# Kernel optimization log

Measured on AMD Instinct MI355X. Metric: run time of the kernel, lower is better.

Reference implementation:

```python
import jax, jax.numpy as jnp
import numpy as np

D_MODEL = 1024
N_HEADS = 16
D_K = D_MODEL // N_HEADS
B, L = 2, 2048


def setup_inputs() -> dict:
    key = jax.random.key(0)
    ks = jax.random.split(key, 13)
    s = 0.02
    inp = {
        'query': jax.random.normal(ks[0], (B, L, D_MODEL), jnp.float32),
        'key': jax.random.normal(ks[1], (B, L, D_MODEL), jnp.float32),
        'value': jax.random.normal(ks[2], (B, L, D_MODEL), jnp.float32),
        'mask': jax.random.randint(ks[3], (1, 1, L, L), 0, 2).astype(bool),
        'W_q': jax.random.normal(ks[4], (D_MODEL, D_MODEL), jnp.float32) * s,
        'b_q': jnp.zeros((D_MODEL,), jnp.float32),
        'W_k': jax.random.normal(ks[5], (D_MODEL, D_MODEL), jnp.float32) * s,
        'b_k': jnp.zeros((D_MODEL,), jnp.float32),
        'W_v': jax.random.normal(ks[6], (D_MODEL, D_MODEL), jnp.float32) * s,
        'b_v': jnp.zeros((D_MODEL,), jnp.float32),
        'W_o': jax.random.normal(ks[7], (D_MODEL, D_MODEL), jnp.float32) * s,
        'b_o': jnp.zeros((D_MODEL,), jnp.float32),
    }
    return inp


def _split_heads(x):
    b, l, _ = x.shape
    return x.reshape(b, l, N_HEADS, D_K).transpose(0, 2, 1, 3)  # [B,H,L,dk]


def reference(query, key, value, mask, W_q, b_q, W_k, b_k, W_v, b_v, W_o, b_o):
    q = _split_heads(query @ W_q + b_q)
    k = _split_heads(key @ W_k + b_k)
    v = _split_heads(value @ W_v + b_v)
    # Unscaled attention logits [B,H,L,L] (NO 1/sqrt(dk))
    logits = jnp.einsum('bhqd,bhkd->bhqk', q, k)
    logits = jnp.where(mask, -jnp.inf, logits)
    w = jax.nn.softmax(logits, axis=-1)
    w = jnp.nan_to_num(w, nan=0.0)  # fully-masked rows -> zeros
    attended = jnp.einsum('bhqk,bhkd->bhqd', w, v)
    # dropout in eval mode = identity; combine heads
    out = attended.transpose(0, 2, 1, 3).reshape(B, L, D_MODEL)
    return out @ W_o + b_o
```

## Files before the change

kernel.cpp:

```cpp
#include <hip/hip_runtime.h>
#include <hip/hip_bf16.h>
#include <stdint.h>


typedef __bf16 bf16;
typedef __bf16 bf16x8 __attribute__((ext_vector_type(8)));
typedef float f32x4 __attribute__((ext_vector_type(4)));

#define AS1 __attribute__((address_space(1)))
#define AS3 __attribute__((address_space(3)))

__device__ __forceinline__ void g2l16(const void* g, void* l) {
    __builtin_amdgcn_global_load_lds((AS1 void*)g, (AS3 void*)l, 16, 0, 0);
}

__device__ __forceinline__ bool lane_masked(unsigned long long m) {
#if __has_builtin(__builtin_amdgcn_inverse_ballot_w64)
    return __builtin_amdgcn_inverse_ballot_w64(m);
#else
    return (m >> (threadIdx.x & 63)) & 1ull;
#endif
}

#define LOG2E 1.44269504088896f

__global__ __launch_bounds__(256) void mdetect_kernel(const unsigned int* __restrict__ w,
                                                      int* __restrict__ flag) {
    int idx = blockIdx.x * 256 + threadIdx.x;
    unsigned v = w[idx];
    int f = 0;
    if (v == 0x3F800000u) f = 2;
    else if (v > 1u) f = 1;
    unsigned long long b1 = __ballot(f & 1);
    unsigned long long b2 = __ballot(f & 2);
    if ((threadIdx.x & 63) == 0) {
        int agg = (b1 ? 1 : 0) | (b2 ? 2 : 0);
        if (agg) atomicOr(flag, agg);
    }
}

__global__ __launch_bounds__(256) void mpack_kernel(const void* __restrict__ mask,
                                                    unsigned long long* __restrict__ mb,
                                                    const int* __restrict__ flag) {
    int idx = blockIdx.x * 256 + threadIdx.x;
    int f = *flag;
    bool v;
    if (f & 2)      v = ((const float*)mask)[idx] != 0.0f;
    else if (f & 1) v = ((const unsigned char*)mask)[idx] != 0;
    else            v = ((const int*)mask)[idx] != 0;
    unsigned long long b = __ballot(v);
    if ((threadIdx.x & 63) == 0) mb[idx >> 6] = b;
}

__global__ __launch_bounds__(256) void rpack_kernel(const unsigned long long* __restrict__ mb,
                                                    unsigned long long* __restrict__ rmb) {
    int task = blockIdx.x * 4 + (threadIdx.x >> 6);
    int qg = task >> 5, kt = task & 31;
    int lane = threadIdx.x & 63, quad = lane >> 4, col = lane & 15;
    #pragma unroll
    for (int r = 0; r < 4; ++r) {
        unsigned long long wrow = mb[(size_t)(qg * 16 + quad * 4 + r) * 32 + kt];
        #pragma unroll
        for (int nt = 0; nt < 4; ++nt) {
            unsigned long long b = __ballot(((wrow >> (nt * 16 + col)) & 1ull) != 0);
            if (lane == 0) rmb[(size_t)task * 16 + r * 4 + nt] = b;
        }
    }
}

__global__ __launch_bounds__(256) void prep_kernel(
    const float* __restrict__ q, const float* __restrict__ k, const float* __restrict__ v,
    bf16* xq, bf16* xk, bf16* xv,
    const float* W0, const float* W1, const float* W2, const float* W3,
    bf16* T0, bf16* T1, bf16* T2, bf16* T3) {
    __shared__ __align__(16) bf16 t[64 * 72];
    int y = blockIdx.y;
    int tid = threadIdx.x;
    if (y < 3) {
        const float* in = (y == 0) ? q : (y == 1) ? k : v;
        bf16* out = (y == 0) ? xq : (y == 1) ? xk : xv;
        int idx = blockIdx.x * 256 + tid;
        float4 vv = ((const float4*)in)[idx];
        __align__(8) bf16 o[4];
        o[0] = (bf16)vv.x; o[1] = (bf16)vv.y; o[2] = (bf16)vv.z; o[3] = (bf16)vv.w;
        *(uint2*)(out + (size_t)idx * 4) = *(const uint2*)o;
        return;
    }
    int bx = blockIdx.x;
    if (bx >= 1024) return;
    const float* W; bf16* T;
    int wi = bx >> 8;
    if (wi == 0)      { W = W0; T = T0; }
    else if (wi == 1) { W = W1; T = T1; }
    else if (wi == 2) { W = W2; T = T2; }
    else              { W = W3; T = T3; }
    int x = bx & 255;
    int tx = x & 15, ty = x >> 4;
    int n0 = tx * 64, k0 = ty * 64;
    #pragma unroll
    for (int rr = 0; rr < 4; ++rr) {
        int idx = rr * 256 + tid;
        int r = idx >> 4, c4 = (idx & 15) * 4;
        float4 vv = *(const float4*)(W + (size_t)(k0 + r) * 1024 + n0 + c4);
        __align__(8) bf16 o[4];
        o[0] = (bf16)vv.x; o[1] = (bf16)vv.y; o[2] = (bf16)vv.z; o[3] = (bf16)vv.w;
        *(uint2*)&t[r * 72 + c4] = *(const uint2*)o;
    }
    __syncthreads();
    #pragma unroll
    for (int rr = 0; rr < 2; ++rr) {
        int idx = rr * 256 + tid;
        int n = idx >> 3, kc = (idx & 7) * 8;
        __align__(16) bf16 o[8];
        #pragma unroll
        for (int j = 0; j < 8; ++j) o[j] = t[(kc + j) * 72 + n];
        *(uint4*)(T + (size_t)(n0 + n) * 1024 + k0 + kc) = *(const uint4*)o;
    }
}

template <int MODE>
__device__ __forceinline__ void gemm128_core(const bf16* __restrict__ A,
                                             const bf16* __restrict__ Bt,
                                             const float* __restrict__ bias,
                                             void* __restrict__ Out, int bm, int bn,
                                             float scale) {
    __shared__ __align__(16) bf16 la[128 * 64];
    __shared__ __align__(16) bf16 lb[128 * 64];
    int tid = threadIdx.x;
    int w = tid >> 6, lane = tid & 63;
    int quad = lane >> 4, col = lane & 15;
    int c7 = col & 7;
    int wm = w >> 1, wn = w & 1;
    int m0 = bm * 128, n0 = bn * 128;
    f32x4 acc[4][4];
    f32x4 z = {0.f, 0.f, 0.f, 0.f};
    #pragma unroll
    for (int i = 0; i < 4; ++i)
        #pragma unroll
        for (int j = 0; j < 4; ++j) acc[i][j] = z;
    int sr = lane >> 3;
    int sg = (lane & 7) ^ sr;
    int swz0 = (quad ^ c7) * 8;
    int swz1 = ((4 + quad) ^ c7) * 8;
    for (int kt = 0; kt < 16; ++kt) {
        int kk = kt * 64;
        __syncthreads();
        #pragma unroll
        for (int i = 0; i < 4; ++i) {
            int ch = w * 4 + i;
            int row = ch * 8 + sr;
            g2l16(A + (size_t)(m0 + row) * 1024 + kk + sg * 8, &la[ch * 512]);
            g2l16(Bt + (size_t)(n0 + row) * 1024 + kk + sg * 8, &lb[ch * 512]);
        }
        __syncthreads();
        bf16x8 af[4][2], bfr[4][2];
        #pragma unroll
        for (int mt = 0; mt < 4; ++mt) {
            af[mt][0] = *(const bf16x8*)&la[(wm * 64 + mt * 16 + col) * 64 + swz0];
            af[mt][1] = *(const bf16x8*)&la[(wm * 64 + mt * 16 + col) * 64 + swz1];
        }
        #pragma unroll
        for (int nt = 0; nt < 4; ++nt) {
            bfr[nt][0] = *(const bf16x8*)&lb[(wn * 64 + nt * 16 + col) * 64 + swz0];
            bfr[nt][1] = *(const bf16x8*)&lb[(wn * 64 + nt * 16 + col) * 64 + swz1];
        }
        #pragma unroll
        for (int mt = 0; mt < 4; ++mt)
            #pragma unroll
            for (int nt = 0; nt < 4; ++nt) {
                acc[mt][nt] = __builtin_amdgcn_mfma_f32_16x16x32_bf16(
                    af[mt][0], bfr[nt][0], acc[mt][nt], 0, 0, 0);
                acc[mt][nt] = __builtin_amdgcn_mfma_f32_16x16x32_bf16(
                    af[mt][1], bfr[nt][1], acc[mt][nt], 0, 0, 0);
            }
    }
    float bia[4];
    #pragma unroll
    for (int nt = 0; nt < 4; ++nt) bia[nt] = bias[n0 + wn * 64 + nt * 16 + col];
    #pragma unroll
    for (int mt = 0; mt < 4; ++mt) {
        #pragma unroll
        for (int nt = 0; nt < 4; ++nt) {
            #pragma unroll
            for (int r = 0; r < 4; ++r) {
                int m = m0 + wm * 64 + mt * 16 + quad * 4 + r;
                int n = n0 + wn * 64 + nt * 16 + col;
                float v = (acc[mt][nt][r] + bia[nt]) * scale;
                if (MODE == 0) {
                    int b = m >> 11, l = m & 2047, h = n >> 6, d = n & 63;
                    ((bf16*)Out)[(((size_t)b * 16 + h) * 2048 + l) * 64 + d] = (bf16)v;
                } else {
                    int b = m >> 11, l = m & 2047, h = n >> 6, d = n & 63;
                    ((bf16*)Out)[(((size_t)b * 16 + h) * 64 + d) * 2048 + l] = (bf16)v;
                }
            }
        }
    }
}

__global__ __launch_bounds__(256) void qkv_kernel(
    const bf16* Xq, const bf16* Xk, const bf16* Xv,
    const bf16* Wq, const bf16* Wk, const bf16* Wv,
    const float* bq, const float* bk, const float* bv,
    bf16* Qh, bf16* Kh, bf16* Vt) {
    int y = blockIdx.y;
    int bm = blockIdx.x >> 3, bn = blockIdx.x & 7;
    if (y == 0)      gemm128_core<0>(Xq, Wq, bq, Qh, bm, bn, LOG2E);
    else if (y == 1) gemm128_core<0>(Xk, Wk, bk, Kh, bm, bn, 1.0f);
    else             gemm128_core<2>(Xv, Wv, bv, Vt, bm, bn, 1.0f);
}

__global__ __launch_bounds__(256) void ogemm_kernel(const bf16* __restrict__ A,
                                                    const bf16* __restrict__ Wt,
                                                    const float* __restrict__ bias,
                                                    float* __restrict__ Out) {
    int bm = blockIdx.x >> 3, bn = blockIdx.x & 7;
    __shared__ __align__(16) bf16 la[64 * 64];
    __shared__ __align__(16) bf16 lb[128 * 64];
    int tid = threadIdx.x;
    int w = tid >> 6, lane = tid & 63;
    int quad = lane >> 4, col = lane & 15;
    int c7 = col & 7;
    int m0 = bm * 64, n0 = bn * 128;
    f32x4 acc[4][2];
    f32x4 z = {0.f, 0.f, 0.f, 0.f};
    #pragma unroll
    for (int i = 0; i < 4; ++i) { acc[i][0] = z; acc[i][1] = z; }
    int sr = lane >> 3;
    int sg = (lane & 7) ^ sr;
    int swz0 = (quad ^ c7) * 8;
    int swz1 = ((4 + quad) ^ c7) * 8;
    for (int kt = 0; kt < 16; ++kt) {
        int kk = kt * 64;
        __syncthreads();
        #pragma unroll
        for (int i = 0; i < 2; ++i) {
            int ch = w * 2 + i;
            g2l16(A + (size_t)(m0 + ch * 8 + sr) * 1024 + kk + sg * 8, &la[ch * 512]);
        }
        #pragma unroll
        for (int i = 0; i < 4; ++i) {
            int ch = w * 4 + i;
            g2l16(Wt + (size_t)(n0 + ch * 8 + sr) * 1024 + kk + sg * 8, &lb[ch * 512]);
        }
        __syncthreads();
        bf16x8 af[4][2], bfr[2][2];
        #pragma unroll
        for (int mt = 0; mt < 4; ++mt) {
            af[mt][0] = *(const bf16x8*)&la[(mt * 16 + col) * 64 + swz0];
            af[mt][1] = *(const bf16x8*)&la[(mt * 16 + col) * 64 + swz1];
        }
        #pragma unroll
        for (int nt = 0; nt < 2; ++nt) {
            bfr[nt][0] = *(const bf16x8*)&lb[(w * 32 + nt * 16 + col) * 64 + swz0];
            bfr[nt][1] = *(const bf16x8*)&lb[(w * 32 + nt * 16 + col) * 64 + swz1];
        }
        #pragma unroll
        for (int mt = 0; mt < 4; ++mt)
            #pragma unroll
            for (int nt = 0; nt < 2; ++nt) {
                acc[mt][nt] = __builtin_amdgcn_mfma_f32_16x16x32_bf16(
                    af[mt][0], bfr[nt][0], acc[mt][nt], 0, 0, 0);
                acc[mt][nt] = __builtin_amdgcn_mfma_f32_16x16x32_bf16(
                    af[mt][1], bfr[nt][1], acc[mt][nt], 0, 0, 0);
            }
    }
    float bia[2];
    bia[0] = bias[n0 + w * 32 + col];
    bia[1] = bias[n0 + w * 32 + 16 + col];
    #pragma unroll
    for (int mt = 0; mt < 4; ++mt)
        #pragma unroll
        for (int nt = 0; nt < 2; ++nt)
            #pragma unroll
            for (int r = 0; r < 4; ++r)
                Out[(size_t)(m0 + mt * 16 + quad * 4 + r) * 1024 +
                    n0 + w * 32 + nt * 16 + col] = acc[mt][nt][r] + bia[nt];
}

__global__ __launch_bounds__(128) void attn_kernel(const bf16* __restrict__ Qh,
                                                   const bf16* __restrict__ Kh,
                                                   const bf16* __restrict__ Vt,
                                                   const unsigned long long* __restrict__ rmb,
                                                   bf16* __restrict__ att) {
    int bh = blockIdx.x, qt = blockIdx.y;
    int b = bh >> 4, h = bh & 15;
    int q0 = qt * 64;
    __shared__ __align__(16) bf16 ks[64 * 64];
    __shared__ __align__(16) bf16 vs[64 * 64];
    __shared__ __align__(16) bf16 ps[2 * 32 * 72];
    int tid = threadIdx.x;
    int w = tid >> 6, lane = tid & 63;
    int quad = lane >> 4, col = lane & 15;
    int c7 = col & 7;
    int sr = lane >> 3;
    int sg = (lane & 7) ^ sr;
    int swz0 = (quad ^ c7) * 8;
    int swz1 = ((4 + quad) ^ c7) * 8;

    int mofs = __builtin_amdgcn_readfirstlane((qt * 4 + w * 2) * 512);

    #pragma unroll
    for (int i = 0; i < 4; ++i) {
        int ch = w * 4 + i;
        g2l16(Qh + ((size_t)bh * 2048 + q0 + ch * 8 + sr) * 64 + sg * 8, &ks[ch * 512]);
    }
    __syncthreads();
    bf16x8 aq[2][2];
    #pragma unroll
    for (int mt = 0; mt < 2; ++mt) {
        aq[mt][0] = *(const bf16x8*)&ks[(w * 32 + mt * 16 + col) * 64 + swz0];
        aq[mt][1] = *(const bf16x8*)&ks[(w * 32 + mt * 16 + col) * 64 + swz1];
    }
    bf16x8 onesf;
    #pragma unroll
    for (int i = 0; i < 8; ++i) onesf[i] = (bf16)1.0f;

    f32x4 z = {0.f, 0.f, 0.f, 0.f};
    f32x4 O[2][4], R[2];
    #pragma unroll
    for (int mt = 0; mt < 2; ++mt) {
        R[mt] = z;
        #pragma unroll
        for (int i = 0; i < 4; ++i) O[mt][i] = z;
    }

    for (int kt = 0; kt < 32; ++kt) {
        __syncthreads();
        #pragma unroll
        for (int i = 0; i < 4; ++i) {
            int ch = w * 4 + i;
            int r = ch * 8 + sr;
            g2l16(Kh + ((size_t)bh * 2048 + kt * 64 + r) * 64 + sg * 8, &ks[ch * 512]);
            g2l16(Vt + ((size_t)bh * 64 + r) * 2048 + kt * 64 + sg * 8, &vs[ch * 512]);
        }
        __syncthreads();

        f32x4 s[2][4];
        #pragma unroll
        for (int nt = 0; nt < 4; ++nt) {
            s[0][nt] = z; s[1][nt] = z;
            bf16x8 bk0 = *(const bf16x8*)&ks[(nt * 16 + col) * 64 + swz0];
            s[0][nt] = __builtin_amdgcn_mfma_f32_16x16x32_bf16(aq[0][0], bk0, s[0][nt], 0, 0, 0);
            s[1][nt] = __builtin_amdgcn_mfma_f32_16x16x32_bf16(aq[1][0], bk0, s[1][nt], 0, 0, 0);
            bf16x8 bk1 = *(const bf16x8*)&ks[(nt * 16 + col) * 64 + swz1];
            s[0][nt] = __builtin_amdgcn_mfma_f32_16x16x32_bf16(aq[0][1], bk1, s[0][nt], 0, 0, 0);
            s[1][nt] = __builtin_amdgcn_mfma_f32_16x16x32_bf16(aq[1][1], bk1, s[1][nt], 0, 0, 0);
        }

        #pragma unroll
        for (int mt = 0; mt < 2; ++mt) {
            const unsigned long long* mw = rmb + mofs + mt * 512 + kt * 16;
            #pragma unroll
            for (int r = 0; r < 4; ++r) {
                #pragma unroll
                for (int nt = 0; nt < 4; ++nt) {
                    float p = __builtin_amdgcn_exp2f(s[mt][nt][r]);
                    if (lane_masked(mw[r * 4 + nt])) p = 0.0f;
                    ps[w * 2304 + (mt * 16 + quad * 4 + r) * 72 + nt * 16 + col] = (bf16)p;
                }
            }
        }

        bf16x8 ap[2][2];
        #pragma unroll
        for (int mt = 0; mt < 2; ++mt) {
            ap[mt][0] = *(const bf16x8*)&ps[w * 2304 + (mt * 16 + col) * 72 + quad * 8];
            ap[mt][1] = *(const bf16x8*)&ps[w * 2304 + (mt * 16 + col) * 72 + 32 + quad * 8];
        }
        #pragma unroll
        for (int dt = 0; dt < 4; ++dt) {
            bf16x8 bv0 = *(const bf16x8*)&vs[(dt * 16 + col) * 64 + swz0];
            O[0][dt] = __builtin_amdgcn_mfma_f32_16x16x32_bf16(ap[0][0], bv0, O[0][dt], 0, 0, 0);
            O[1][dt] = __builtin_amdgcn_mfma_f32_16x16x32_bf16(ap[1][0], bv0, O[1][dt], 0, 0, 0);
            bf16x8 bv1 = *(const bf16x8*)&vs[(dt * 16 + col) * 64 + swz1];
            O[0][dt] = __builtin_amdgcn_mfma_f32_16x16x32_bf16(ap[0][1], bv1, O[0][dt], 0, 0, 0);
            O[1][dt] = __builtin_amdgcn_mfma_f32_16x16x32_bf16(ap[1][1], bv1, O[1][dt], 0, 0, 0);
        }
        #pragma unroll
        for (int mt = 0; mt < 2; ++mt) {
            R[mt] = __builtin_amdgcn_mfma_f32_16x16x32_bf16(ap[mt][0], onesf, R[mt], 0, 0, 0);
            R[mt] = __builtin_amdgcn_mfma_f32_16x16x32_bf16(ap[mt][1], onesf, R[mt], 0, 0, 0);
        }
    }

    #pragma unroll
    for (int mt = 0; mt < 2; ++mt) {
        #pragma unroll
        for (int r = 0; r < 4; ++r) {
            float rsv = R[mt][r];
            float inv = (rsv > 0.f) ? 1.0f / rsv : 0.f;
            int qg = q0 + w * 32 + mt * 16 + quad * 4 + r;
            #pragma unroll
            for (int dt = 0; dt < 4; ++dt) {
                float ov = O[mt][dt][r] * inv;
                att[((size_t)b * 2048 + qg) * 1024 + h * 64 + dt * 16 + col] = (bf16)ov;
            }
        }
    }
}

extern "C" void kernel_launch(void* const* d_in, const int* in_sizes, int n_in,
                              void* d_out, int out_size, void* d_ws, size_t ws_size,
                              hipStream_t stream) {
    (void)in_sizes; (void)n_in; (void)out_size; (void)ws_size;
    const float* query = (const float*)d_in[0];
    const float* key_  = (const float*)d_in[1];
    const float* value = (const float*)d_in[2];
    const void*  mask  = d_in[3];
    const float* W_q = (const float*)d_in[4];
    const float* b_q = (const float*)d_in[5];
    const float* W_k = (const float*)d_in[6];
    const float* b_k = (const float*)d_in[7];
    const float* W_v = (const float*)d_in[8];
    const float* b_v = (const float*)d_in[9];
    const float* W_o = (const float*)d_in[10];
    const float* b_o = (const float*)d_in[11];

    char* ws = (char*)d_ws;
    bf16* Xq  = (bf16*)(ws + 0);
    bf16* Xk  = (bf16*)(ws + 8388608);
    bf16* Xv  = (bf16*)(ws + 16777216);
    bf16* Wtq = (bf16*)(ws + 25165824);
    bf16* Wtk = (bf16*)(ws + 27262976);
    bf16* Wtv = (bf16*)(ws + 29360128);
    bf16* Wto = (bf16*)(ws + 31457280);
    bf16* Qh  = (bf16*)(ws + 33554432);
    bf16* Kh  = (bf16*)(ws + 41943040);
    bf16* Vt  = (bf16*)(ws + 50331648);
    bf16* att = (bf16*)(ws + 58720256);
    unsigned long long* mb  = (unsigned long long*)(ws + 67108864);
    unsigned long long* rmb = (unsigned long long*)(ws + 67633152);
    int* flag = (int*)(ws + 68157440);

    hipMemsetAsync(flag, 0, 4, stream);
    mdetect_kernel<<<4096, 256, 0, stream>>>((const unsigned int*)mask, flag);
    mpack_kernel<<<16384, 256, 0, stream>>>(mask, mb, flag);
    rpack_kernel<<<1024, 256, 0, stream>>>(mb, rmb);

    prep_kernel<<<dim3(4096, 4), 256, 0, stream>>>(query, key_, value, Xq, Xk, Xv,
                                                   W_q, W_k, W_v, W_o,
                                                   Wtq, Wtk, Wtv, Wto);

    qkv_kernel<<<dim3(256, 3), 256, 0, stream>>>(Xq, Xk, Xv, Wtq, Wtk, Wtv,
                                                 b_q, b_k, b_v, Qh, Kh, Vt);
    attn_kernel<<<dim3(32, 32), 128, 0, stream>>>(Qh, Kh, Vt, rmb, att);
    ogemm_kernel<<<512, 256, 0, stream>>>(att, Wto, b_o, (float*)d_out);
}
```

Baseline: 279.7 us.

## Split attention into single-wave blocks with waitcnt sync and swizzled P buffer

The attention kernel now uses one 64-thread wave per block, covering 32 query rows, and launches twice as many blocks. With a single wave, __syncthreads is replaced by explicit s_waitcnt vmcnt/lgkmcnt fences, and the P scratch tile drops its padding in favour of an XOR swizzle. The goal is to remove barrier overhead and raise occupancy. The cost is that each K/V tile is now loaded by every 32-row block, doubling K/V global/L2 traffic.

```diff
diff --git a/kernel.cpp b/kernel.cpp
--- a/kernel.cpp
+++ b/kernel.cpp
@@ -278,19 +278,18 @@
                     n0 + w * 32 + nt * 16 + col] = acc[mt][nt][r] + bia[nt];
 }
 
-__global__ __launch_bounds__(128) void attn_kernel(const bf16* __restrict__ Qh,
-                                                   const bf16* __restrict__ Kh,
-                                                   const bf16* __restrict__ Vt,
-                                                   const unsigned long long* __restrict__ rmb,
-                                                   bf16* __restrict__ att) {
-    int bh = blockIdx.x, qt = blockIdx.y;
+__global__ __launch_bounds__(64, 2) void attn_kernel(const bf16* __restrict__ Qh,
+                                                     const bf16* __restrict__ Kh,
+                                                     const bf16* __restrict__ Vt,
+                                                     const unsigned long long* __restrict__ rmb,
+                                                     bf16* __restrict__ att) {
+    int bh = blockIdx.x, qtn = blockIdx.y;
     int b = bh >> 4, h = bh & 15;
-    int q0 = qt * 64;
+    int q0 = qtn * 32;
     __shared__ __align__(16) bf16 ks[64 * 64];
     __shared__ __align__(16) bf16 vs[64 * 64];
-    __shared__ __align__(16) bf16 ps[2 * 32 * 72];
-    int tid = threadIdx.x;
-    int w = tid >> 6, lane = tid & 63;
+    __shared__ __align__(16) bf16 ps[32 * 64];
+    int lane = threadIdx.x;
     int quad = lane >> 4, col = lane & 15;
     int c7 = col & 7;
     int sr = lane >> 3;
@@ -298,19 +297,18 @@
     int swz0 = (quad ^ c7) * 8;
     int swz1 = ((4 + quad) ^ c7) * 8;
 
-    int mofs = __builtin_amdgcn_readfirstlane((qt * 4 + w * 2) * 512);
-
-    #pragma unroll
-    for (int i = 0; i < 4; ++i) {
-        int ch = w * 4 + i;
-        g2l16(Qh + ((size_t)bh * 2048 + q0 + ch * 8 + sr) * 64 + sg * 8, &ks[ch * 512]);
-    }
-    __syncthreads();
+    int mofs = __builtin_amdgcn_readfirstlane(qtn * 1024);
+
+    #pragma unroll
+    for (int i = 0; i < 4; ++i)
+        g2l16(Qh + ((size_t)bh * 2048 + q0 + i * 8 + sr) * 64 + sg * 8, &ks[i * 512]);
+    asm volatile("s_waitcnt vmcnt(0)" ::: "memory");
+    __builtin_amdgcn_sched_barrier(0);
     bf16x8 aq[2][2];
     #pragma unroll
     for (int mt = 0; mt < 2; ++mt) {
-        aq[mt][0] = *(const bf16x8*)&ks[(w * 32 + mt * 16 + col) * 64 + swz0];
-        aq[mt][1] = *(const bf16x8*)&ks[(w * 32 + mt * 16 + col) * 64 + swz1];
+        aq[mt][0] = *(const bf16x8*)&ks[(mt * 16 + col) * 64 + swz0];
+        aq[mt][1] = *(const bf16x8*)&ks[(mt * 16 + col) * 64 + swz1];
     }
     bf16x8 onesf;
     #pragma unroll
@@ -326,15 +324,16 @@
     }
 
     for (int kt = 0; kt < 32; ++kt) {
-        __syncthreads();
-        #pragma unroll
-        for (int i = 0; i < 4; ++i) {
-            int ch = w * 4 + i;
-            int r = ch * 8 + sr;
-            g2l16(Kh + ((size_t)bh * 2048 + kt * 64 + r) * 64 + sg * 8, &ks[ch * 512]);
-            g2l16(Vt + ((size_t)bh * 64 + r) * 2048 + kt * 64 + sg * 8, &vs[ch * 512]);
-        }
-        __syncthreads();
+        asm volatile("s_waitcnt lgkmcnt(0)" ::: "memory");
+        __builtin_amdgcn_sched_barrier(0);
+        #pragma unroll
+        for (int i = 0; i < 8; ++i) {
+            int r = i * 8 + sr;
+            g2l16(Kh + ((size_t)bh * 2048 + kt * 64 + r) * 64 + sg * 8, &ks[i * 512]);
+            g2l16(Vt + ((size_t)bh * 64 + r) * 2048 + kt * 64 + sg * 8, &vs[i * 512]);
+        }
+        asm volatile("s_waitcnt vmcnt(0)" ::: "memory");
+        __builtin_amdgcn_sched_barrier(0);
 
         f32x4 s[2][4];
         #pragma unroll
@@ -353,11 +352,13 @@
             const unsigned long long* mw = rmb + mofs + mt * 512 + kt * 16;
             #pragma unroll
             for (int r = 0; r < 4; ++r) {
+                int row = mt * 16 + quad * 4 + r;
+                int xs = ((quad * 4 + r) & 7) << 3;
                 #pragma unroll
                 for (int nt = 0; nt < 4; ++nt) {
                     float p = __builtin_amdgcn_exp2f(s[mt][nt][r]);
                     if (lane_masked(mw[r * 4 + nt])) p = 0.0f;
-                    ps[w * 2304 + (mt * 16 + quad * 4 + r) * 72 + nt * 16 + col] = (bf16)p;
+                    ps[row * 64 + ((nt * 16 + col) ^ xs)] = (bf16)p;
                 }
             }
         }
@@ -365,8 +366,8 @@
         bf16x8 ap[2][2];
         #pragma unroll
         for (int mt = 0; mt < 2; ++mt) {
-            ap[mt][0] = *(const bf16x8*)&ps[w * 2304 + (mt * 16 + col) * 72 + quad * 8];
-            ap[mt][1] = *(const bf16x8*)&ps[w * 2304 + (mt * 16 + col) * 72 + 32 + quad * 8];
+            ap[mt][0] = *(const bf16x8*)&ps[(mt * 16 + col) * 64 + swz0];
+            ap[mt][1] = *(const bf16x8*)&ps[(mt * 16 + col) * 64 + swz1];
         }
         #pragma unroll
         for (int dt = 0; dt < 4; ++dt) {
@@ -390,7 +391,7 @@
         for (int r = 0; r < 4; ++r) {
             float rsv = R[mt][r];
             float inv = (rsv > 0.f) ? 1.0f / rsv : 0.f;
-            int qg = q0 + w * 32 + mt * 16 + quad * 4 + r;
+            int qg = q0 + mt * 16 + quad * 4 + r;
             #pragma unroll
             for (int dt = 0; dt < 4; ++dt) {
                 float ov = O[mt][dt][r] * inv;
@@ -444,6 +445,6 @@
 
     qkv_kernel<<<dim3(256, 3), 256, 0, stream>>>(Xq, Xk, Xv, Wtq, Wtk, Wtv,
                                                  b_q, b_k, b_v, Qh, Kh, Vt);
-    attn_kernel<<<dim3(32, 32), 128, 0, stream>>>(Qh, Kh, Vt, rmb, att);
+    attn_kernel<<<dim3(32, 64), 64, 0, stream>>>(Qh, Kh, Vt, rmb, att);
     ogemm_kernel<<<512, 256, 0, stream>>>(att, Wto, b_o, (float*)d_out);
 }
```

Measured after the change: 302.2 us. +8.1%, slower.

## Fold mask packing into prep kernel, reading mask as 32-bit words

Applied to the files above, without the earlier changes.

Removes the mask dtype detection, intermediate bit-pack and repack kernels, plus the memset. A new y==4 slice of prep_kernel reads the mask directly as 32-bit words and ballots it into the per-tile rmb layout. This saves three launches and the intermediate mb buffer traffic. It assumes the mask is stored as 4-byte elements and drops support for byte or float masks.

```diff
diff --git a/kernel.cpp b/kernel.cpp
--- a/kernel.cpp
+++ b/kernel.cpp
@@ -24,55 +24,12 @@
 
 #define LOG2E 1.44269504088896f
 
-__global__ __launch_bounds__(256) void mdetect_kernel(const unsigned int* __restrict__ w,
-                                                      int* __restrict__ flag) {
-    int idx = blockIdx.x * 256 + threadIdx.x;
-    unsigned v = w[idx];
-    int f = 0;
-    if (v == 0x3F800000u) f = 2;
-    else if (v > 1u) f = 1;
-    unsigned long long b1 = __ballot(f & 1);
-    unsigned long long b2 = __ballot(f & 2);
-    if ((threadIdx.x & 63) == 0) {
-        int agg = (b1 ? 1 : 0) | (b2 ? 2 : 0);
-        if (agg) atomicOr(flag, agg);
-    }
-}
-
-__global__ __launch_bounds__(256) void mpack_kernel(const void* __restrict__ mask,
-                                                    unsigned long long* __restrict__ mb,
-                                                    const int* __restrict__ flag) {
-    int idx = blockIdx.x * 256 + threadIdx.x;
-    int f = *flag;
-    bool v;
-    if (f & 2)      v = ((const float*)mask)[idx] != 0.0f;
-    else if (f & 1) v = ((const unsigned char*)mask)[idx] != 0;
-    else            v = ((const int*)mask)[idx] != 0;
-    unsigned long long b = __ballot(v);
-    if ((threadIdx.x & 63) == 0) mb[idx >> 6] = b;
-}
-
-__global__ __launch_bounds__(256) void rpack_kernel(const unsigned long long* __restrict__ mb,
-                                                    unsigned long long* __restrict__ rmb) {
-    int task = blockIdx.x * 4 + (threadIdx.x >> 6);
-    int qg = task >> 5, kt = task & 31;
-    int lane = threadIdx.x & 63, quad = lane >> 4, col = lane & 15;
-    #pragma unroll
-    for (int r = 0; r < 4; ++r) {
-        unsigned long long wrow = mb[(size_t)(qg * 16 + quad * 4 + r) * 32 + kt];
-        #pragma unroll
-        for (int nt = 0; nt < 4; ++nt) {
-            unsigned long long b = __ballot(((wrow >> (nt * 16 + col)) & 1ull) != 0);
-            if (lane == 0) rmb[(size_t)task * 16 + r * 4 + nt] = b;
-        }
-    }
-}
-
 __global__ __launch_bounds__(256) void prep_kernel(
     const float* __restrict__ q, const float* __restrict__ k, const float* __restrict__ v,
     bf16* xq, bf16* xk, bf16* xv,
     const float* W0, const float* W1, const float* W2, const float* W3,
-    bf16* T0, bf16* T1, bf16* T2, bf16* T3) {
+    bf16* T0, bf16* T1, bf16* T2, bf16* T3,
+    const unsigned int* __restrict__ mask, unsigned long long* __restrict__ rmb) {
     __shared__ __align__(16) bf16 t[64 * 72];
     int y = blockIdx.y;
     int tid = threadIdx.x;
@@ -84,6 +41,25 @@
         __align__(8) bf16 o[4];
         o[0] = (bf16)vv.x; o[1] = (bf16)vv.y; o[2] = (bf16)vv.z; o[3] = (bf16)vv.w;
         *(uint2*)(out + (size_t)idx * 4) = *(const uint2*)o;
+        return;
+    }
+    if (y == 4) {
+        int bx = blockIdx.x;
+        if (bx >= 1024) return;
+        int task = bx * 4 + (tid >> 6);
+        int qg = task >> 5, kt = task & 31;
+        int lane = tid & 63, quad = lane >> 4, col = lane & 15;
+        int row0 = qg * 16 + quad * 4;
+        int c0 = kt * 64 + col;
+        #pragma unroll
+        for (int r = 0; r < 4; ++r) {
+            const unsigned int* mrow = mask + (size_t)(row0 + r) * 2048;
+            #pragma unroll
+            for (int nt = 0; nt < 4; ++nt) {
+                unsigned long long b = __ballot(mrow[c0 + nt * 16] != 0u);
+                if (lane == 0) rmb[(size_t)task * 16 + r * 4 + nt] = b;
+            }
+        }
         return;
     }
     int bx = blockIdx.x;
@@ -429,18 +405,12 @@
     bf16* Kh  = (bf16*)(ws + 41943040);
     bf16* Vt  = (bf16*)(ws + 50331648);
     bf16* att = (bf16*)(ws + 58720256);
-    unsigned long long* mb  = (unsigned long long*)(ws + 67108864);
     unsigned long long* rmb = (unsigned long long*)(ws + 67633152);
-    int* flag = (int*)(ws + 68157440);
-
-    hipMemsetAsync(flag, 0, 4, stream);
-    mdetect_kernel<<<4096, 256, 0, stream>>>((const unsigned int*)mask, flag);
-    mpack_kernel<<<16384, 256, 0, stream>>>(mask, mb, flag);
-    rpack_kernel<<<1024, 256, 0, stream>>>(mb, rmb);
-
-    prep_kernel<<<dim3(4096, 4), 256, 0, stream>>>(query, key_, value, Xq, Xk, Xv,
+
+    prep_kernel<<<dim3(4096, 5), 256, 0, stream>>>(query, key_, value, Xq, Xk, Xv,
                                                    W_q, W_k, W_v, W_o,
-                                                   Wtq, Wtk, Wtv, Wto);
+                                                   Wtq, Wtk, Wtv, Wto,
+                                                   (const unsigned int*)mask, rmb);
 
     qkv_kernel<<<dim3(256, 3), 256, 0, stream>>>(Xq, Xk, Xv, Wtq, Wtk, Wtv,
                                                  b_q, b_k, b_v, Qh, Kh, Vt);
```

Result: faster. 266.5 us (-4.7%).
